# Performance work log

Hardware: AMD Instinct MI355X
Metric: run time of the kernel (lower is better)

Reference implementation:

```python
import jax, jax.numpy as jnp
import numpy as np

NUM_EMB = 8192
EMB_DIM = 32
LATENT = 1024
COMMIT = 0.25
CB_COST = 1.0


def _l2norm(x, eps=1e-12):
    # matches torch F.normalize: x / max(||x||, eps)
    n = jnp.sqrt(jnp.sum(x * x, axis=-1, keepdims=True))
    return x / jnp.maximum(n, eps)


def setup_inputs() -> dict:
    key = jax.random.key(0)
    k = jax.random.split(key, 6)
    B = 32768
    s_in = 1.0 / np.sqrt(LATENT)
    s_out = 1.0 / np.sqrt(EMB_DIM)
    return {
        "z_e": jax.random.normal(k[0], (B, LATENT), jnp.float32),
        "in_w": jax.random.uniform(k[1], (EMB_DIM, LATENT), jnp.float32, -s_in, s_in),
        "in_b": jax.random.uniform(k[2], (EMB_DIM,), jnp.float32, -s_in, s_in),
        "out_w": jax.random.uniform(k[3], (LATENT, EMB_DIM), jnp.float32, -s_out, s_out),
        "out_b": jax.random.uniform(k[4], (LATENT,), jnp.float32, -s_out, s_out),
        "codebook": jax.random.normal(k[5], (NUM_EMB, EMB_DIM), jnp.float32),
    }


def reference(z_e, in_w, in_b, out_w, out_b, codebook):
    # in_proj: [B, LATENT] -> [B, EMB_DIM]
    ze = z_e @ in_w.T + in_b
    zn = _l2norm(ze)                      # [B, E]
    wn = _l2norm(codebook)                # [Z, E]
    # squared euclidean distance between normalized vectors
    dist = (jnp.sum(zn * zn, axis=1, keepdims=True)
            - 2.0 * (zn @ wn.T)
            + jnp.sum(wn * wn, axis=1))   # [B, Z]
    idx = jnp.argmin(dist, axis=1)        # [B]
    z_q = codebook[idx]                   # [B, E] (unnormalized codebook lookup)
    enc_loss = jnp.mean((ze - jax.lax.stop_gradient(z_q)) ** 2)
    cb_loss = jnp.mean((z_q - jax.lax.stop_gradient(ze)) ** 2)
    loss = CB_COST * cb_loss + COMMIT * enc_loss
    # straight-through estimator
    z_st = ze + jax.lax.stop_gradient(z_q - ze)
    out = z_st @ out_w.T + out_b          # [B, LATENT]
    return out, loss, enc_loss, cb_loss, idx, ze
```

## Files before the change

kernel.cpp:

```cpp
#include <hip/hip_runtime.h>
#include <hip/hip_bf16.h>

#define B_SZ    32768
#define LAT     1024
#define EMB     32
#define ZCB     8192
#define NSPL    8
#define CPS     (ZCB / NSPL)
#define RESC_CAP 32768
#define EPS_MARGIN 2e-4f

#define OFF_LOSS  ((size_t)B_SZ * LAT)
#define OFF_ENC   (OFF_LOSS + 1)
#define OFF_CB    (OFF_LOSS + 2)
#define OFF_IDX   (OFF_LOSS + 3)
#define OFF_ZE    (OFF_IDX + B_SZ)

#define WS_PZE    0
#define WS_PB1    0
#define WS_PB2    262144
#define WS_PL15   524288
#define WS_CAND   786432
#define WS_OTH    819200
#define WS_ZEA    2097152
#define WS_ZNPK   3145728
#define WS_WPK    4194304
#define WS_IDXT   4456448
#define WS_CNT    4489216
#define WS_LIST   4489217
#define WS_LPART  4521985

typedef float  f32x4  __attribute__((ext_vector_type(4)));
typedef short  short8 __attribute__((ext_vector_type(8)));

__device__ __forceinline__ unsigned short f2bf(float x) {
    unsigned u = __float_as_uint(x);
    u += 0x7FFF + ((u >> 16) & 1);
    return (unsigned short)(u >> 16);
}
__device__ __forceinline__ float bf2f(unsigned short h) {
    return __uint_as_float(((unsigned)h) << 16);
}

__global__ __launch_bounds__(256) void knorm(const float* __restrict__ cb,
                                             short* __restrict__ wpk) {
    int e = threadIdx.x;
    int r = threadIdx.y;
    int row = blockIdx.x * 8 + r;
    float v = cb[row * EMB + e];
    float s = v * v;
    #pragma unroll
    for (int m = 16; m >= 1; m >>= 1) s += __shfl_xor(s, m, 64);
    float n = fmaxf(sqrtf(s), 1e-12f);
    float w = v / n;
    unsigned short h = f2bf(w);
    unsigned short l = f2bf(w - bf2f(h));
    wpk[row * 64 + e]      = (short)h;
    wpk[row * 64 + 32 + e] = (short)l;
}

#define KZB 64
#define KZS 68
__global__ __launch_bounds__(256) void kze2(const float* __restrict__ z_e,
                                            const float* __restrict__ in_w,
                                            float* __restrict__ pze) {
    __shared__ float zs[64 * KZS];
    __shared__ float wt[KZB * 32];
    int tid = threadIdx.x;
    size_t row0 = (size_t)blockIdx.x * 64;
    int ks = blockIdx.y;
    int rs = tid >> 2;
    int eg = tid & 3;
    int E  = eg * 8;

    float acc[8];
    #pragma unroll
    for (int j = 0; j < 8; ++j) acc[j] = 0.f;

    for (int c = 0; c < 512 / KZB; ++c) {
        int kb = ks * 512 + c * KZB;
        __syncthreads();
        #pragma unroll
        for (int i = 0; i < 4; ++i) {
            int t = tid + i * 256;
            int r = t >> 4, c4 = t & 15;
            float4 v = *(const float4*)(z_e + (row0 + r) * LAT + kb + c4 * 4);
            *(float4*)&zs[r * KZS + c4 * 4] = v;
        }
        #pragma unroll
        for (int i = 0; i < 2; ++i) {
            int t = tid + i * 256;
            int e = t >> 4, k4 = t & 15;
            float4 v = *(const float4*)(in_w + (size_t)e * LAT + kb + k4 * 4);
            float vv[4] = {v.x, v.y, v.z, v.w};
            #pragma unroll
            for (int j = 0; j < 4; ++j) {
                int k = k4 * 4 + j;
                wt[k * 32 + (e ^ ((k & 7) << 2))] = vv[j];
            }
        }
        __syncthreads();
        #pragma unroll 4
        for (int kq = 0; kq < KZB / 4; ++kq) {
            int k0 = kq * 4;
            float4 za = *(const float4*)&zs[rs * KZS + k0];
            float zav[4] = {za.x, za.y, za.z, za.w};
            #pragma unroll
            for (int i = 0; i < 4; ++i) {
                int k = k0 + i;
                int sw = (k & 7) << 2;
                float4 w0 = *(const float4*)&wt[k * 32 + (E ^ sw)];
                float4 w1 = *(const float4*)&wt[k * 32 + ((E + 4) ^ sw)];
                float wa[8] = {w0.x, w0.y, w0.z, w0.w, w1.x, w1.y, w1.z, w1.w};
                #pragma unroll
                for (int j = 0; j < 8; ++j)
                    acc[j] = fmaf(zav[i], wa[j], acc[j]);
            }
        }
    }
    size_t rb = (size_t)ks * B_SZ + row0;
    float* p0 = pze + (rb + rs) * EMB + E;
    *(float4*)p0       = make_float4(acc[0], acc[1], acc[2], acc[3]);
    *(float4*)(p0 + 4) = make_float4(acc[4], acc[5], acc[6], acc[7]);
}

__global__ __launch_bounds__(256) void kprep(const float* __restrict__ pze,
                                             const float* __restrict__ in_b,
                                             float* __restrict__ ze_out,
                                             float* __restrict__ ze_a,
                                             short* __restrict__ znpk) {
    int tid = threadIdx.x;
    size_t row = (size_t)blockIdx.x * 64 + (tid >> 2);
    int eg = tid & 3;
    const float* p0 = pze + row * 32 + eg * 8;
    const float* p1 = p0 + (size_t)B_SZ * 32;
    float4 a0 = *(const float4*)p0, a1 = *(const float4*)(p0 + 4);
    float4 b0 = *(const float4*)p1, b1 = *(const float4*)(p1 + 4);
    float4 c0 = *(const float4*)(in_b + eg * 8), c1 = *(const float4*)(in_b + eg * 8 + 4);
    float v[8];
    v[0] = a0.x + b0.x + c0.x; v[1] = a0.y + b0.y + c0.y;
    v[2] = a0.z + b0.z + c0.z; v[3] = a0.w + b0.w + c0.w;
    v[4] = a1.x + b1.x + c1.x; v[5] = a1.y + b1.y + c1.y;
    v[6] = a1.z + b1.z + c1.z; v[7] = a1.w + b1.w + c1.w;
    float nn = 0.f;
    #pragma unroll
    for (int i = 0; i < 8; ++i) nn = fmaf(v[i], v[i], nn);
    nn += __shfl_xor(nn, 1, 64);
    nn += __shfl_xor(nn, 2, 64);
    float n = fmaxf(sqrtf(nn), 1e-12f);

    *(float4*)(ze_a + row * 32 + eg * 8)     = make_float4(v[0], v[1], v[2], v[3]);
    *(float4*)(ze_a + row * 32 + eg * 8 + 4) = make_float4(v[4], v[5], v[6], v[7]);
    #pragma unroll
    for (int i = 0; i < 8; ++i) ze_out[row * 32 + eg * 8 + i] = v[i];

    short8 hv, lv;
    #pragma unroll
    for (int i = 0; i < 8; ++i) {
        float x = v[i] / n;
        unsigned short h = f2bf(x);
        unsigned short l = f2bf(x - bf2f(h));
        hv[i] = (short)h; lv[i] = (short)l;
    }
    *(short8*)(znpk + row * 64 + eg * 8)      = hv;
    *(short8*)(znpk + row * 64 + 32 + eg * 8) = lv;
}

__global__ __launch_bounds__(256) void kdistM(const short* __restrict__ znpk,
                                              const short* __restrict__ wpk,
                                              float* __restrict__ pb1,
                                              float* __restrict__ pb2,
                                              int*   __restrict__ pl15) {
    int tid = threadIdx.x;
    int wave = tid >> 6, l = tid & 63;
    int l15 = l & 15, g = l >> 4;
    size_t rowbase = (size_t)blockIdx.x * 256 + wave * 64;
    int s = blockIdx.y;

    short8 zh[4], zl[4];
    #pragma unroll
    for (int rt = 0; rt < 4; ++rt) {
        const short8* p = (const short8*)(znpk + (rowbase + rt * 16 + l15) * 64 + g * 8);
        zh[rt] = p[0];
        zl[rt] = p[4];
    }
    f32x4 zero4 = {0.f, 0.f, 0.f, 0.f};
    float bb1[16];
    #pragma unroll
    for (int i = 0; i < 16; ++i) bb1[i] = -1e30f;

    const short* wbase = wpk + ((size_t)s * CPS + l15) * 64 + g * 8;
    const short8* wp0 = (const short8*)wbase;
    short8 bh = wp0[0];
    short8 bl = wp0[4];
    for (int t = 0; t < CPS / 16; ++t) {
        short8 nbh = bh, nbl = bl;
        if (t + 1 < CPS / 16) {
            const short8* wn = (const short8*)(wbase + (size_t)(t + 1) * 1024);
            nbh = wn[0];
            nbl = wn[4];
        }
        #pragma unroll
        for (int rt = 0; rt < 4; ++rt) {
            f32x4 c1 = __builtin_amdgcn_mfma_f32_16x16x32_bf16(zh[rt], bh, zero4, 0, 0, 0);
            f32x4 c2 = __builtin_amdgcn_mfma_f32_16x16x32_bf16(zh[rt], bl, zero4, 0, 0, 0);
            c2 = __builtin_amdgcn_mfma_f32_16x16x32_bf16(zl[rt], bh, c2, 0, 0, 0);
            #pragma unroll
            for (int r = 0; r < 4; ++r) {
                int slot = rt * 4 + r;
                bb1[slot] = fmaxf(bb1[slot], c1[r] + c2[r]);
            }
        }
        bh = nbh; bl = nbl;
    }
    #pragma unroll
    for (int slot = 0; slot < 16; ++slot) {
        float B1 = bb1[slot], B2 = -1e30f;
        int ID = l15;
        #pragma unroll
        for (int m = 1; m <= 8; m <<= 1) {
            float ob1 = __shfl_xor(B1, m, 64);
            float ob2 = __shfl_xor(B2, m, 64);
            int   oid = __shfl_xor(ID, m, 64);
            float mn = fminf(B1, ob1);
            B2 = fmaxf(fmaxf(B2, ob2), mn);
            bool take = (ob1 > B1) || (ob1 == B1 && oid < ID);
            B1 = take ? ob1 : B1;
            ID = take ? oid : ID;
        }
        if (l15 == 0) {
            size_t row = rowbase + (size_t)(slot >> 2) * 16 + g * 4 + (slot & 3);
            pb1[(size_t)s * B_SZ + row] = B1;
            pb2[(size_t)s * B_SZ + row] = B2;
            pl15[(size_t)s * B_SZ + row] = ID;
        }
    }
}

__global__ __launch_bounds__(256) void kmergeArg(const float* __restrict__ pb1,
                                                 const float* __restrict__ pb2,
                                                 const int* __restrict__ pl15,
                                                 int* __restrict__ cand,
                                                 float* __restrict__ oth,
                                                 int* __restrict__ cnt) {
    if (blockIdx.x == 0 && threadIdx.x == 0) *cnt = 0;
    int row = blockIdx.x * 256 + threadIdx.x;
    float best1 = pb1[row], best2 = pb2[row];
    int c = pl15[row], wsn = 0;
    #pragma unroll
    for (int s = 1; s < NSPL; ++s) {
        float b  = pb1[(size_t)s * B_SZ + row];
        float sb = pb2[(size_t)s * B_SZ + row];
        int   li = pl15[(size_t)s * B_SZ + row];
        float mn = fminf(best1, b);
        best2 = fmaxf(fmaxf(best2, sb), mn);
        if (b > best1) { best1 = b; c = li; wsn = s; }
    }
    cand[row] = wsn * 16 + c;
    oth[row] = best2;
}

__global__ __launch_bounds__(256) void krecover(const float* __restrict__ ze_a,
                                                const float* __restrict__ cb,
                                                const int* __restrict__ cand,
                                                const float* __restrict__ oth,
                                                int* __restrict__ idxt,
                                                int* __restrict__ cnt,
                                                int* __restrict__ list) {
    int tid = threadIdx.x;
    int l = tid & 63;
    int gl = l & 7;
    int gj = l >> 3;
    int row = (blockIdx.x * 256 + tid) >> 6;
    int c = cand[row];
    int s = c >> 4, lc = c & 15;
    float4 z = *(const float4*)(ze_a + (size_t)row * 32 + gl * 4);
    float zz = fmaf(z.x, z.x, fmaf(z.y, z.y, fmaf(z.z, z.z, z.w * z.w)));
    zz += __shfl_xor(zz, 1, 64);
    zz += __shfl_xor(zz, 2, 64);
    zz += __shfl_xor(zz, 4, 64);
    float zinv = 1.f / fmaxf(sqrtf(zz), 1e-12f);
    z.x *= zinv; z.y *= zinv; z.z *= zinv; z.w *= zinv;

    float best = -1e30f; int bi = 0;
    #pragma unroll
    for (int b = 0; b < CPS / 16 / 8; ++b) {
        int t = b * 8 + gj;
        int j = s * CPS + t * 16 + lc;
        float4 w = *(const float4*)(cb + (size_t)j * 32 + gl * 4);
        float w2 = fmaf(w.x, w.x, fmaf(w.y, w.y, fmaf(w.z, w.z, w.w * w.w)));
        float dt = fmaf(z.x, w.x, fmaf(z.y, w.y, fmaf(z.z, w.z, z.w * w.w)));
        w2 += __shfl_xor(w2, 1, 64); dt += __shfl_xor(dt, 1, 64);
        w2 += __shfl_xor(w2, 2, 64); dt += __shfl_xor(dt, 2, 64);
        w2 += __shfl_xor(w2, 4, 64); dt += __shfl_xor(dt, 4, 64);
        float inv = 1.f / fmaxf(sqrtf(w2), 1e-12f);
        float m = dt * inv - 0.5f * (w2 * inv * inv);
        if (m > best || (m == best && j < bi)) { best = m; bi = j; }
    }
    #pragma unroll
    for (int mk = 8; mk <= 32; mk <<= 1) {
        float ob = __shfl_xor(best, mk, 64);
        int   oi = __shfl_xor(bi, mk, 64);
        bool take = (ob > best) || (ob == best && oi < bi);
        best = take ? ob : best;
        bi   = take ? oi : bi;
    }
    if (l == 0) {
        idxt[row] = bi;
        if (best - (oth[row] - 0.5f) < EPS_MARGIN) {
            int p = atomicAdd(cnt, 1);
            if (p < RESC_CAP) list[p] = row;
        }
    }
}

__global__ __launch_bounds__(256) void krescore(const float* __restrict__ ze_a,
                                                const float* __restrict__ cb,
                                                int* __restrict__ idxt,
                                                const int* __restrict__ cnt,
                                                const int* __restrict__ list) {
    __shared__ float bvs[4];
    __shared__ int   bis[4];
    int tid = threadIdx.x;
    int wave = tid >> 6, l = tid & 63;
    int gl = l & 7;
    int gj = l >> 3;
    int n = *cnt; if (n > RESC_CAP) n = RESC_CAP;
    for (int ii = blockIdx.x; ii < n; ii += gridDim.x) {
        int row = list[ii];
        float4 z = *(const float4*)(ze_a + (size_t)row * 32 + gl * 4);
        float zz = fmaf(z.x, z.x, fmaf(z.y, z.y, fmaf(z.z, z.z, z.w * z.w)));
        zz += __shfl_xor(zz, 1, 64);
        zz += __shfl_xor(zz, 2, 64);
        zz += __shfl_xor(zz, 4, 64);
        float zinv = 1.f / fmaxf(sqrtf(zz), 1e-12f);
        z.x *= zinv; z.y *= zinv; z.z *= zinv; z.w *= zinv;

        float best = -1e30f; int bi = 0;
        int jbase = wave * 2048 + gj;
        for (int b = 0; b < 32; ++b) {
            float w2v[8], dtv[8];
            #pragma unroll
            for (int cc = 0; cc < 8; ++cc) {
                int j = jbase + (b * 8 + cc) * 8;
                float4 w = *(const float4*)(cb + (size_t)j * 32 + gl * 4);
                w2v[cc] = fmaf(w.x, w.x, fmaf(w.y, w.y, fmaf(w.z, w.z, w.w * w.w)));
                dtv[cc] = fmaf(z.x, w.x, fmaf(z.y, w.y, fmaf(z.z, w.z, z.w * w.w)));
            }
            #pragma unroll
            for (int cc = 0; cc < 8; ++cc) {
                w2v[cc] += __shfl_xor(w2v[cc], 1, 64);
                dtv[cc] += __shfl_xor(dtv[cc], 1, 64);
            }
            #pragma unroll
            for (int cc = 0; cc < 8; ++cc) {
                w2v[cc] += __shfl_xor(w2v[cc], 2, 64);
                dtv[cc] += __shfl_xor(dtv[cc], 2, 64);
            }
            #pragma unroll
            for (int cc = 0; cc < 8; ++cc) {
                w2v[cc] += __shfl_xor(w2v[cc], 4, 64);
                dtv[cc] += __shfl_xor(dtv[cc], 4, 64);
            }
            #pragma unroll
            for (int cc = 0; cc < 8; ++cc) {
                int j = jbase + (b * 8 + cc) * 8;
                float inv = 1.f / fmaxf(sqrtf(w2v[cc]), 1e-12f);
                float m = dtv[cc] * inv - 0.5f * (w2v[cc] * inv * inv);
                if (m > best || (m == best && j < bi)) { best = m; bi = j; }
            }
        }
        #pragma unroll
        for (int mk = 8; mk <= 32; mk <<= 1) {
            float ob = __shfl_xor(best, mk, 64);
            int   oi = __shfl_xor(bi, mk, 64);
            bool take = (ob > best) || (ob == best && oi < bi);
            best = take ? ob : best;
            bi   = take ? oi : bi;
        }
        if (l == 0) { bvs[wave] = best; bis[wave] = bi; }
        __syncthreads();
        if (tid == 0) {
            float B = bvs[0]; int I = bis[0];
            #pragma unroll
            for (int w2i = 1; w2i < 4; ++w2i) {
                float ob = bvs[w2i]; int oi = bis[w2i];
                if (ob > B || (ob == B && oi < I)) { B = ob; I = oi; }
            }
            idxt[row] = I;
        }
        __syncthreads();
    }
}

__global__ __launch_bounds__(256) void kfinal(const int* __restrict__ idxt,
                                              const float* __restrict__ ze,
                                              const float* __restrict__ cb,
                                              float* __restrict__ out_idx,
                                              float* __restrict__ lpart) {
    int tid = threadIdx.x;
    int row = blockIdx.x * 256 + tid;
    int bidx = idxt[row];
    out_idx[row] = (float)bidx;

    const float4* zq4 = (const float4*)(cb + (size_t)bidx * EMB);
    const float4* ze4 = (const float4*)(ze + (size_t)row * EMB);
    float sq = 0.f;
    #pragma unroll
    for (int i = 0; i < 8; ++i) {
        float4 q = zq4[i], z = ze4[i];
        float dx = z.x - q.x, dy = z.y - q.y, dz = z.z - q.z, dw = z.w - q.w;
        sq += (dx * dx + dy * dy) + (dz * dz + dw * dw);
    }
    #pragma unroll
    for (int m = 1; m <= 32; m <<= 1) sq += __shfl_xor(sq, m, 64);
    __shared__ float red[4];
    if ((tid & 63) == 0) red[tid >> 6] = sq;
    __syncthreads();
    if (tid == 0) lpart[blockIdx.x] = (red[0] + red[1]) + (red[2] + red[3]);
}

__global__ void kloss(const float* __restrict__ lpart, float* __restrict__ dout) {
    float v = lpart[threadIdx.x];
    #pragma unroll
    for (int m = 1; m <= 32; m <<= 1) v += __shfl_xor(v, m, 64);
    __shared__ float tmp[2];
    if ((threadIdx.x & 63) == 0) tmp[threadIdx.x >> 6] = v;
    __syncthreads();
    if (threadIdx.x == 0) {
        float enc = (tmp[0] + tmp[1]) / (float)(B_SZ * EMB);
        dout[OFF_LOSS] = 1.0f * enc + 0.25f * enc;
        dout[OFF_ENC]  = enc;
        dout[OFF_CB]   = enc;
    }
}

__global__ __launch_bounds__(256) void kout(const float* __restrict__ ze_a,
                                            const int* __restrict__ idxt,
                                            const float* __restrict__ cb,
                                            const float* __restrict__ out_w,
                                            const float* __restrict__ out_b,
                                            float* __restrict__ out) {
    __shared__ float zsh[128 * EMB];
    __shared__ int ish[128];
    int tid = threadIdx.x;
    int col = blockIdx.x * 512 + tid * 2;
    size_t row0 = (size_t)blockIdx.y * 128;
    if (tid < 128) ish[tid] = idxt[row0 + tid];
    __syncthreads();
    #pragma unroll
    for (int i = 0; i < 4; ++i) {
        int flat = i * 256 + tid;
        int r = flat >> 3, q = flat & 7;
        float4 zv = *(const float4*)(ze_a + (row0 + r) * EMB + q * 4);
        float4 qv = *(const float4*)(cb + (size_t)ish[r] * EMB + q * 4);
        float4 o;
        o.x = zv.x + (qv.x - zv.x); o.y = zv.y + (qv.y - zv.y);
        o.z = zv.z + (qv.z - zv.z); o.w = zv.w + (qv.w - zv.w);
        *(float4*)&zsh[r * EMB + q * 4] = o;
    }
    float wa[32], wb[32];
    {
        const float4* wa4 = (const float4*)(out_w + (size_t)col * EMB);
        const float4* wb4 = (const float4*)(out_w + (size_t)(col + 1) * EMB);
        #pragma unroll
        for (int i = 0; i < 8; ++i) {
            float4 a = wa4[i]; wa[4*i]=a.x; wa[4*i+1]=a.y; wa[4*i+2]=a.z; wa[4*i+3]=a.w;
            float4 b = wb4[i]; wb[4*i]=b.x; wb[4*i+1]=b.y; wb[4*i+2]=b.z; wb[4*i+3]=b.w;
        }
    }
    float b0 = out_b[col], b1 = out_b[col + 1];
    __syncthreads();
    for (int rr = 0; rr < 128; ++rr) {
        const float4* zr4 = (const float4*)(zsh + rr * EMB);
        float a0 = b0, a1 = b1;
        #pragma unroll
        for (int q = 0; q < 8; ++q) {
            float4 z = zr4[q];
            a0 = fmaf(z.x, wa[4*q],   a0); a1 = fmaf(z.x, wb[4*q],   a1);
            a0 = fmaf(z.y, wa[4*q+1], a0); a1 = fmaf(z.y, wb[4*q+1], a1);
            a0 = fmaf(z.z, wa[4*q+2], a0); a1 = fmaf(z.z, wb[4*q+2], a1);
            a0 = fmaf(z.w, wa[4*q+3], a0); a1 = fmaf(z.w, wb[4*q+3], a1);
        }
        float2 o; o.x = a0; o.y = a1;
        *(float2*)(out + (row0 + rr) * LAT + col) = o;
    }
}

extern "C" void kernel_launch(void* const* d_in, const int* in_sizes, int n_in,
                              void* d_out, int out_size, void* d_ws, size_t ws_size,
                              hipStream_t stream) {
    const float* z_e   = (const float*)d_in[0];
    const float* in_w  = (const float*)d_in[1];
    const float* in_b  = (const float*)d_in[2];
    const float* out_w = (const float*)d_in[3];
    const float* out_b = (const float*)d_in[4];
    const float* cb    = (const float*)d_in[5];

    float* out = (float*)d_out;
    float* ws  = (float*)d_ws;
    float* pze   = ws + WS_PZE;
    float* pb1   = ws + WS_PB1;
    float* pb2   = ws + WS_PB2;
    int*   pl15  = (int*)(ws + WS_PL15);
    int*   cand  = (int*)(ws + WS_CAND);
    float* oth   = ws + WS_OTH;
    float* ze_a  = ws + WS_ZEA;
    short* znpk  = (short*)(ws + WS_ZNPK);
    short* wpk   = (short*)(ws + WS_WPK);
    int*   idxt  = (int*)(ws + WS_IDXT);
    int*   cnt   = (int*)(ws + WS_CNT);
    int*   list  = (int*)(ws + WS_LIST);
    float* lpart = ws + WS_LPART;

    knorm    <<<dim3(ZCB / 8), dim3(32, 8), 0, stream>>>(cb, wpk);
    kze2     <<<dim3(B_SZ / 64, 2), 256, 0, stream>>>(z_e, in_w, pze);
    kprep    <<<dim3(B_SZ / 64), 256, 0, stream>>>(pze, in_b, out + OFF_ZE, ze_a, znpk);
    kdistM   <<<dim3(B_SZ / 256, NSPL), 256, 0, stream>>>(znpk, wpk, pb1, pb2, pl15);
    kmergeArg<<<dim3(B_SZ / 256), 256, 0, stream>>>(pb1, pb2, pl15, cand, oth, cnt);
    krecover <<<dim3(B_SZ / 4), 256, 0, stream>>>(ze_a, cb, cand, oth, idxt, cnt, list);
    krescore <<<dim3(512), 256, 0, stream>>>(ze_a, cb, idxt, cnt, list);
    kfinal   <<<dim3(B_SZ / 256), 256, 0, stream>>>(idxt, ze_a, cb, out + OFF_IDX, lpart);
    kloss    <<<1, 128, 0, stream>>>(lpart, out);
    kout     <<<dim3(2, B_SZ / 128), 256, 0, stream>>>(ze_a, idxt, cb, out_w, out_b, out);
}
```

Baseline: 274.3 us.

## Stage codebook chunks in swizzled LDS with double buffering in distance kernel

Measured after the change: 260.1 us. 5.2% less time.

```diff
diff --git a/kernel.cpp b/kernel.cpp
--- a/kernel.cpp
+++ b/kernel.cpp
@@ -171,6 +171,7 @@
                                               float* __restrict__ pb1,
                                               float* __restrict__ pb2,
                                               int*   __restrict__ pl15) {
+    __shared__ short wch[2][128 * 64];
     int tid = threadIdx.x;
     int wave = tid >> 6, l = tid & 63;
     int l15 = l & 15, g = l >> 4;
@@ -189,29 +190,53 @@
     #pragma unroll
     for (int i = 0; i < 16; ++i) bb1[i] = -1e30f;
 
-    const short* wbase = wpk + ((size_t)s * CPS + l15) * 64 + g * 8;
-    const short8* wp0 = (const short8*)wbase;
-    short8 bh = wp0[0];
-    short8 bl = wp0[4];
-    for (int t = 0; t < CPS / 16; ++t) {
-        short8 nbh = bh, nbl = bl;
-        if (t + 1 < CPS / 16) {
-            const short8* wn = (const short8*)(wbase + (size_t)(t + 1) * 1024);
-            nbh = wn[0];
-            nbl = wn[4];
-        }
-        #pragma unroll
-        for (int rt = 0; rt < 4; ++rt) {
-            f32x4 c1 = __builtin_amdgcn_mfma_f32_16x16x32_bf16(zh[rt], bh, zero4, 0, 0, 0);
-            f32x4 c2 = __builtin_amdgcn_mfma_f32_16x16x32_bf16(zh[rt], bl, zero4, 0, 0, 0);
-            c2 = __builtin_amdgcn_mfma_f32_16x16x32_bf16(zl[rt], bh, c2, 0, 0, 0);
-            #pragma unroll
-            for (int r = 0; r < 4; ++r) {
-                int slot = rt * 4 + r;
-                bb1[slot] = fmaxf(bb1[slot], c1[r] + c2[r]);
-            }
-        }
-        bh = nbh; bl = nbl;
+    int sw = (l15 & 7) << 4;
+    int bhoff = ((g * 16) ^ sw) >> 1;
+    int bloff = ((64 + g * 16) ^ sw) >> 1;
+
+    const short* wsrc = wpk + (size_t)s * CPS * 64;
+
+    #pragma unroll
+    for (int i = 0; i < 4; ++i) {
+        int t = tid + i * 256;
+        int code = t >> 3, slot = t & 7;
+        short8 v = *(const short8*)(wsrc + (size_t)code * 64 + slot * 8);
+        int doff = (slot * 16) ^ ((code & 7) << 4);
+        *(short8*)&wch[0][code * 64 + (doff >> 1)] = v;
+    }
+    __syncthreads();
+
+    for (int c = 0; c < 8; ++c) {
+        if (c + 1 < 8) {
+            const short* src = wsrc + (size_t)(c + 1) * 128 * 64;
+            #pragma unroll
+            for (int i = 0; i < 4; ++i) {
+                int t = tid + i * 256;
+                int code = t >> 3, slot = t & 7;
+                short8 v = *(const short8*)(src + (size_t)code * 64 + slot * 8);
+                int doff = (slot * 16) ^ ((code & 7) << 4);
+                *(short8*)&wch[(c + 1) & 1][code * 64 + (doff >> 1)] = v;
+            }
+        }
+        const short* W = &wch[c & 1][0];
+        #pragma unroll
+        for (int tt = 0; tt < 8; ++tt) {
+            const short* rowp = W + (tt * 16 + l15) * 64;
+            short8 bh = *(const short8*)(rowp + bhoff);
+            short8 bl = *(const short8*)(rowp + bloff);
+            #pragma unroll
+            for (int rt = 0; rt < 4; ++rt) {
+                f32x4 acc = __builtin_amdgcn_mfma_f32_16x16x32_bf16(zh[rt], bh, zero4, 0, 0, 0);
+                acc = __builtin_amdgcn_mfma_f32_16x16x32_bf16(zl[rt], bh, acc, 0, 0, 0);
+                acc = __builtin_amdgcn_mfma_f32_16x16x32_bf16(zh[rt], bl, acc, 0, 0, 0);
+                #pragma unroll
+                for (int r = 0; r < 4; ++r) {
+                    int slot = rt * 4 + r;
+                    bb1[slot] = fmaxf(bb1[slot], acc[r]);
+                }
+            }
+        }
+        __syncthreads();
     }
     #pragma unroll
     for (int slot = 0; slot < 16; ++slot) {
```
